# Performance work log

Hardware: AMD Instinct MI355X
Metric: run time of the kernel (lower is better)

The kernel has to match this reference:

```python
import jax, jax.numpy as jnp
import numpy as np

D_IN, L, D, K, N_CLASSES = 1024, 512, 384, 1, 2

def setup_inputs() -> dict:
    key = jax.random.key(0)
    ks = jax.random.split(key, 11)
    x = jax.random.normal(ks[0], (2, 40000, D_IN), dtype=jnp.float32)
    # Linear params stored as [in, out]; xavier-normal-ish scale
    def w(k, i, o):
        return jax.random.normal(k, (i, o), dtype=jnp.float32) * jnp.sqrt(2.0 / (i + o))
    return {
        "x": x,
        "Wf": w(ks[1], D_IN, L), "bf": jnp.zeros((L,), jnp.float32),
        "Wa": w(ks[2], L, D),    "ba": jnp.zeros((D,), jnp.float32),
        "Wb": w(ks[3], L, D),    "bb": jnp.zeros((D,), jnp.float32),
        "Wc": w(ks[4], D, K),    "bc": jnp.zeros((K,), jnp.float32),
        "Wcls": w(ks[5], L * K, N_CLASSES), "bcls": jnp.zeros((N_CLASSES,), jnp.float32),
    }

def reference(x, Wf, bf, Wa, ba, Wb, bb, Wc, bc, Wcls, bcls):
    # feature embed: Linear + ReLU  (mil_norm=None -> Identity norms)
    h = jax.nn.relu(jnp.einsum('bnd,de->bne', x, Wf) + bf)   # [B,N,L]
    # gated attention
    a = jnp.tanh(jnp.einsum('bnl,ld->bnd', h, Wa) + ba)      # [B,N,D]
    g = jax.nn.sigmoid(jnp.einsum('bnl,ld->bnd', h, Wb) + bb)
    s = jnp.einsum('bnd,dk->bnk', a * g, Wc) + bc            # [B,N,K]
    A = jax.nn.softmax(jnp.swapaxes(s, -1, -2), axis=-1)     # [B,K,N]
    pooled = jnp.einsum('bkn,bnl->bkl', A, h)                # [B,K,L]
    logits = jnp.squeeze(pooled, 1) @ Wcls + bcls            # [B,n_classes]
    return logits
```

## Files before the change

### kernel.cpp

```cpp
#include <hip/hip_runtime.h>
#include <cstdint>

typedef _Float16 f16;
typedef __attribute__((ext_vector_type(8))) _Float16 half8;
typedef __attribute__((ext_vector_type(4))) float floatx4;

#define NB      40000
#define M_TOTAL 80000
#define DIN     1024
#define LDIM    512
#define NBLK    1250
#define BPB     625

__global__ void k_prep(const float* __restrict__ Wf, const float* __restrict__ Wa,
                       const float* __restrict__ Wb,
                       f16* __restrict__ packedF, f16* __restrict__ packedAB)
{
    const int gid = blockIdx.x * 256 + threadIdx.x;
    if (gid < 65536) {
        const int lq = gid & 3, n = (gid >> 2) & 511, kb = gid >> 11;
        const int kbase = kb * 32 + lq * 8;
        half8 v;
        #pragma unroll
        for (int j = 0; j < 8; ++j) v[j] = (f16)Wf[(kbase + j) * 512 + n];
        *(half8*)&packedF[(long)gid * 8] = v;
    } else if (gid < 65536 + 49152) {
        const int g = gid - 65536;
        const int kb = g / 3072;
        const int rem = g - kb * 3072;
        const int c = rem >> 2, lq = rem & 3;
        const int d = ((c >> 5) << 4) + (c & 15);
        const int type = (c >> 4) & 1;
        const float* src = type ? Wb : Wa;
        const int kbase = kb * 32 + lq * 8;
        half8 v;
        #pragma unroll
        for (int j = 0; j < 8; ++j) v[j] = (f16)src[(kbase + j) * 384 + d];
        *(half8*)&packedAB[(long)g * 8] = v;
    }
}

__device__ inline float fast_sigmoid(float xx) { return 1.0f / (1.0f + __expf(-xx)); }
__device__ inline float fast_tanh(float xx) {
    float e = __expf(-2.0f * fabsf(xx));
    float r = (1.0f - e) / (1.0f + e);
    return xx >= 0.0f ? r : -r;
}

__global__ __launch_bounds__(512, 4) void k_fused(
    const float* __restrict__ x, const f16* __restrict__ packedF,
    const f16* __restrict__ packedAB,
    const float* __restrict__ bf, const float* __restrict__ ba,
    const float* __restrict__ bb, const float* __restrict__ Wc,
    float* __restrict__ partial_pool, float* __restrict__ partial_denom)
{
    __shared__ __align__(16) f16 Hs[64][520];
    __shared__ __align__(16) f16 As[64][72];
    __shared__ float wbuf[64];
    const int tid = threadIdx.x;
    const int w = tid >> 6, lane = tid & 63, lr = lane & 15, lq = lane >> 4;
    const long row0 = (long)blockIdx.x * 64;
    const int sr = tid >> 3, st = (tid & 7) * 8;
    const float* xp = x + (row0 + sr) * DIN + st;
    if (tid < 64) wbuf[tid] = 0.0f;

    floatx4 acc[4][4] = {};
    float4 xa = *(const float4*)xp;
    float4 xb = *(const float4*)(xp + 4);
    for (int kt = 0; kt < 16; ++kt) {
        __syncthreads();
        {
            half8 hv;
            hv[0]=(f16)xa.x; hv[1]=(f16)xa.y; hv[2]=(f16)xa.z; hv[3]=(f16)xa.w;
            hv[4]=(f16)xb.x; hv[5]=(f16)xb.y; hv[6]=(f16)xb.z; hv[7]=(f16)xb.w;
            *(half8*)&As[sr][st] = hv;
        }
        __syncthreads();
        if (kt < 15) {
            const float* q = xp + (kt + 1) * 64;
            xa = *(const float4*)q;
            xb = *(const float4*)(q + 4);
        }
        #pragma unroll
        for (int kq = 0; kq < 2; ++kq) {
            const int kb = kt * 2 + kq;
            half8 bfr[4];
            #pragma unroll
            for (int tj = 0; tj < 4; ++tj)
                bfr[tj] = *(const half8*)&packedF[(long)((kb * 512 + w * 64 + tj * 16 + lr) << 5) + lq * 8];
            half8 af[4];
            #pragma unroll
            for (int ti = 0; ti < 4; ++ti)
                af[ti] = *(const half8*)&As[ti * 16 + lr][kq * 32 + lq * 8];
            #pragma unroll
            for (int tj = 0; tj < 4; ++tj)
                #pragma unroll
                for (int ti = 0; ti < 4; ++ti)
                    acc[ti][tj] = __builtin_amdgcn_mfma_f32_16x16x32_f16(af[ti], bfr[tj], acc[ti][tj], 0, 0, 0);
        }
    }
    #pragma unroll
    for (int tj = 0; tj < 4; ++tj) {
        const int col = w * 64 + tj * 16 + lr;
        const float bias = bf[col];
        #pragma unroll
        for (int ti = 0; ti < 4; ++ti)
            #pragma unroll
            for (int r = 0; r < 4; ++r)
                Hs[ti * 16 + lq * 4 + r][col] = (f16)fmaxf(acc[ti][tj][r] + bias, 0.0f);
    }
    __syncthreads();

    floatx4 acc2[4][6] = {};
    for (int kb = 0; kb < 16; ++kb) {
        half8 af[4];
        #pragma unroll
        for (int ti = 0; ti < 4; ++ti)
            af[ti] = *(const half8*)&Hs[ti * 16 + lr][kb * 32 + lq * 8];
        #pragma unroll
        for (int tj = 0; tj < 6; ++tj) {
            half8 bfr = *(const half8*)&packedAB[(long)((kb * 768 + w * 96 + tj * 16 + lr) << 5) + lq * 8];
            #pragma unroll
            for (int ti = 0; ti < 4; ++ti)
                acc2[ti][tj] = __builtin_amdgcn_mfma_f32_16x16x32_f16(af[ti], bfr, acc2[ti][tj], 0, 0, 0);
        }
    }
    float sp[4][4] = {};
    #pragma unroll
    for (int u = 0; u < 3; ++u) {
        const int d = w * 48 + u * 16 + lr;
        const float biasA = ba[d], biasB = bb[d], wcv = Wc[d];
        #pragma unroll
        for (int ti = 0; ti < 4; ++ti)
            #pragma unroll
            for (int r = 0; r < 4; ++r) {
                const float av = fast_tanh(acc2[ti][2 * u][r] + biasA);
                const float gv = fast_sigmoid(acc2[ti][2 * u + 1][r] + biasB);
                sp[ti][r] += av * gv * wcv;
            }
    }
    #pragma unroll
    for (int m = 1; m < 16; m <<= 1)
        #pragma unroll
        for (int ti = 0; ti < 4; ++ti)
            #pragma unroll
            for (int r = 0; r < 4; ++r)
                sp[ti][r] += __shfl_xor(sp[ti][r], m, 64);
    if (lr == 0) {
        #pragma unroll
        for (int ti = 0; ti < 4; ++ti)
            #pragma unroll
            for (int r = 0; r < 4; ++r)
                atomicAdd(&wbuf[ti * 16 + lq * 4 + r], sp[ti][r]);
    }
    __syncthreads();
    if (tid < 64) wbuf[tid] = __expf(wbuf[tid]);
    __syncthreads();

    {
        const int c = tid;
        float pacc = 0.0f;
        #pragma unroll 8
        for (int n = 0; n < 64; ++n)
            pacc += wbuf[n] * (float)Hs[n][c];
        partial_pool[(long)blockIdx.x * 512 + c] = pacc;
    }
    if (w == 0) {
        float dsum = wbuf[lane];
        #pragma unroll
        for (int o = 32; o > 0; o >>= 1) dsum += __shfl_xor(dsum, o, 64);
        if (lane == 0) partial_denom[blockIdx.x] = dsum;
    }
}

__global__ __launch_bounds__(512) void k_reduce(
    const float* __restrict__ pp, const float* __restrict__ pd,
    const float* __restrict__ Wcls, const float* __restrict__ bcls,
    float* __restrict__ out)
{
    __shared__ float pooled[512];
    __shared__ float dsh[8];
    const int b = blockIdx.x, tid = threadIdx.x;
    float acc = 0.0f;
    const float* base = pp + (long)b * BPB * 512 + tid;
    for (int i = 0; i < BPB; ++i) acc += base[(long)i * 512];
    pooled[tid] = acc;
    float d = 0.0f;
    for (int i = tid; i < BPB; i += 512) d += pd[b * BPB + i];
    #pragma unroll
    for (int o = 32; o > 0; o >>= 1) d += __shfl_xor(d, o, 64);
    if ((tid & 63) == 0) dsh[tid >> 6] = d;
    __syncthreads();
    const float denom = dsh[0] + dsh[1] + dsh[2] + dsh[3] + dsh[4] + dsh[5] + dsh[6] + dsh[7];
    if (tid < 128) {
        const int cls = tid >> 6, ln = tid & 63;
        float sum = 0.0f;
        #pragma unroll
        for (int t = 0; t < 8; ++t)
            sum += pooled[t * 64 + ln] * Wcls[(t * 64 + ln) * 2 + cls];
        #pragma unroll
        for (int o = 32; o > 0; o >>= 1) sum += __shfl_xor(sum, o, 64);
        if (ln == 0) out[b * 2 + cls] = sum / denom + bcls[cls];
    }
}

extern "C" void kernel_launch(void* const* d_in, const int* in_sizes, int n_in,
                              void* d_out, int out_size, void* d_ws, size_t ws_size,
                              hipStream_t stream)
{
    const float* x    = (const float*)d_in[0];
    const float* Wf   = (const float*)d_in[1];
    const float* bf   = (const float*)d_in[2];
    const float* Wa   = (const float*)d_in[3];
    const float* ba   = (const float*)d_in[4];
    const float* Wb   = (const float*)d_in[5];
    const float* bb   = (const float*)d_in[6];
    const float* Wc   = (const float*)d_in[7];
    const float* Wcls = (const float*)d_in[9];
    const float* bcls = (const float*)d_in[10];
    float* out = (float*)d_out;

    char* w = (char*)d_ws;
    f16*   packedF  = (f16*)(w);
    f16*   packedAB = (f16*)(w + 1048576);
    float* ppool    = (float*)(w + 1835008);
    float* pdenom   = (float*)(w + 4395008);

    k_prep  <<<448, 256, 0, stream>>>(Wf, Wa, Wb, packedF, packedAB);
    k_fused <<<NBLK, 512, 0, stream>>>(x, packedF, packedAB, bf, ba, bb, Wc, ppool, pdenom);
    k_reduce<<<2, 512, 0, stream>>>(ppool, pdenom, Wcls, bcls, out);
}
```

Baseline: 712.9 us.

## Swizzle LDS tiles, widen K-step to 128, split final reduction into two stages

Replaces padded LDS arrays with XOR-swizzled layouts for the x tile and the H tile to avoid bank conflicts without padding. The x staging tile doubles to 128 columns, halving the number of barrier-separated K iterations. wbuf now aliases the A tile. The single 2-block final reduction over 625 partials per batch is split into a 32-block first pass and a small second pass, adding a launch in exchange for more parallelism. The second-stage buffers reuse the packedF workspace region, which k_fused no longer needs by then.

Result: faster. 690.3 us (-3.2%).

```diff
diff --git a/kernel.cpp b/kernel.cpp
--- a/kernel.cpp
+++ b/kernel.cpp
@@ -11,6 +11,8 @@
 #define LDIM    512
 #define NBLK    1250
 #define BPB     625
+#define NCHUNK  16
+#define RCHUNK  40
 
 __global__ void k_prep(const float* __restrict__ Wf, const float* __restrict__ Wa,
                        const float* __restrict__ Wb,
@@ -54,36 +56,46 @@
     const float* __restrict__ bb, const float* __restrict__ Wc,
     float* __restrict__ partial_pool, float* __restrict__ partial_denom)
 {
-    __shared__ __align__(16) f16 Hs[64][520];
-    __shared__ __align__(16) f16 As[64][72];
-    __shared__ float wbuf[64];
+    __shared__ __align__(16) f16 Hs[64][512];
+    __shared__ __align__(16) f16 As[64][128];
+    float* wbuf = (float*)&As[0][0];
+
     const int tid = threadIdx.x;
     const int w = tid >> 6, lane = tid & 63, lr = lane & 15, lq = lane >> 4;
     const long row0 = (long)blockIdx.x * 64;
-    const int sr = tid >> 3, st = (tid & 7) * 8;
-    const float* xp = x + (row0 + sr) * DIN + st;
-    if (tid < 64) wbuf[tid] = 0.0f;
+    const int sr = tid >> 3;
+    const int sc = (tid & 7) << 4;
+    const int swzw = (sr & 7) << 3;
+    const int swzr = (lr & 7) << 3;
+    const float* xp = x + (row0 + sr) * DIN + sc;
 
     floatx4 acc[4][4] = {};
-    float4 xa = *(const float4*)xp;
-    float4 xb = *(const float4*)(xp + 4);
-    for (int kt = 0; kt < 16; ++kt) {
+    float4 xr0 = *(const float4*)xp;
+    float4 xr1 = *(const float4*)(xp + 4);
+    float4 xr2 = *(const float4*)(xp + 8);
+    float4 xr3 = *(const float4*)(xp + 12);
+    for (int kt = 0; kt < 8; ++kt) {
+        if (kt) __syncthreads();
+        {
+            half8 v0, v1;
+            v0[0]=(f16)xr0.x; v0[1]=(f16)xr0.y; v0[2]=(f16)xr0.z; v0[3]=(f16)xr0.w;
+            v0[4]=(f16)xr1.x; v0[5]=(f16)xr1.y; v0[6]=(f16)xr1.z; v0[7]=(f16)xr1.w;
+            v1[0]=(f16)xr2.x; v1[1]=(f16)xr2.y; v1[2]=(f16)xr2.z; v1[3]=(f16)xr2.w;
+            v1[4]=(f16)xr3.x; v1[5]=(f16)xr3.y; v1[6]=(f16)xr3.z; v1[7]=(f16)xr3.w;
+            *(half8*)&As[sr][sc ^ swzw] = v0;
+            *(half8*)&As[sr][(sc + 8) ^ swzw] = v1;
+        }
         __syncthreads();
-        {
-            half8 hv;
-            hv[0]=(f16)xa.x; hv[1]=(f16)xa.y; hv[2]=(f16)xa.z; hv[3]=(f16)xa.w;
-            hv[4]=(f16)xb.x; hv[5]=(f16)xb.y; hv[6]=(f16)xb.z; hv[7]=(f16)xb.w;
-            *(half8*)&As[sr][st] = hv;
-        }
-        __syncthreads();
-        if (kt < 15) {
-            const float* q = xp + (kt + 1) * 64;
-            xa = *(const float4*)q;
-            xb = *(const float4*)(q + 4);
-        }
-        #pragma unroll
-        for (int kq = 0; kq < 2; ++kq) {
-            const int kb = kt * 2 + kq;
+        if (kt < 7) {
+            const float* q = xp + (kt + 1) * 128;
+            xr0 = *(const float4*)q;
+            xr1 = *(const float4*)(q + 4);
+            xr2 = *(const float4*)(q + 8);
+            xr3 = *(const float4*)(q + 12);
+        }
+        #pragma unroll
+        for (int kq = 0; kq < 4; ++kq) {
+            const int kb = kt * 4 + kq;
             half8 bfr[4];
             #pragma unroll
             for (int tj = 0; tj < 4; ++tj)
@@ -91,7 +103,7 @@
             half8 af[4];
             #pragma unroll
             for (int ti = 0; ti < 4; ++ti)
-                af[ti] = *(const half8*)&As[ti * 16 + lr][kq * 32 + lq * 8];
+                af[ti] = *(const half8*)&As[ti * 16 + lr][(kq * 32 + lq * 8) ^ swzr];
             #pragma unroll
             for (int tj = 0; tj < 4; ++tj)
                 #pragma unroll
@@ -106,9 +118,13 @@
         #pragma unroll
         for (int ti = 0; ti < 4; ++ti)
             #pragma unroll
-            for (int r = 0; r < 4; ++r)
-                Hs[ti * 16 + lq * 4 + r][col] = (f16)fmaxf(acc[ti][tj][r] + bias, 0.0f);
-    }
+            for (int r = 0; r < 4; ++r) {
+                const int row = ti * 16 + lq * 4 + r;
+                Hs[row][col ^ ((row & 7) << 3)] = (f16)fmaxf(acc[ti][tj][r] + bias, 0.0f);
+            }
+    }
+    __syncthreads();
+    if (tid < 64) wbuf[tid] = 0.0f;
     __syncthreads();
 
     floatx4 acc2[4][6] = {};
@@ -116,7 +132,7 @@
         half8 af[4];
         #pragma unroll
         for (int ti = 0; ti < 4; ++ti)
-            af[ti] = *(const half8*)&Hs[ti * 16 + lr][kb * 32 + lq * 8];
+            af[ti] = *(const half8*)&Hs[ti * 16 + lr][(kb * 32 + lq * 8) ^ swzr];
         #pragma unroll
         for (int tj = 0; tj < 6; ++tj) {
             half8 bfr = *(const half8*)&packedAB[(long)((kb * 768 + w * 96 + tj * 16 + lr) << 5) + lq * 8];
@@ -162,7 +178,7 @@
         float pacc = 0.0f;
         #pragma unroll 8
         for (int n = 0; n < 64; ++n)
-            pacc += wbuf[n] * (float)Hs[n][c];
+            pacc += wbuf[n] * (float)Hs[n][c ^ ((n & 7) << 3)];
         partial_pool[(long)blockIdx.x * 512 + c] = pacc;
     }
     if (w == 0) {
@@ -173,8 +189,32 @@
     }
 }
 
-__global__ __launch_bounds__(512) void k_reduce(
+__global__ __launch_bounds__(512) void k_reduce1(
     const float* __restrict__ pp, const float* __restrict__ pd,
+    float* __restrict__ pp2, float* __restrict__ pd2)
+{
+    __shared__ float dsh[8];
+    const int b = blockIdx.x >> 4, chunk = blockIdx.x & 15;
+    const int tid = threadIdx.x;
+    const int r0 = chunk * RCHUNK;
+    const int rows = (BPB - r0 < RCHUNK) ? (BPB - r0) : RCHUNK;
+    const float* base = pp + ((long)b * BPB + r0) * 512 + tid;
+    float acc = 0.0f;
+    for (int i = 0; i < rows; ++i) acc += base[(long)i * 512];
+    pp2[((long)b * NCHUNK + chunk) * 512 + tid] = acc;
+    float d = 0.0f;
+    for (int i = tid; i < rows; i += 512) d += pd[b * BPB + r0 + i];
+    #pragma unroll
+    for (int o = 32; o > 0; o >>= 1) d += __shfl_xor(d, o, 64);
+    if ((tid & 63) == 0) dsh[tid >> 6] = d;
+    __syncthreads();
+    if (tid == 0)
+        pd2[b * NCHUNK + chunk] = dsh[0] + dsh[1] + dsh[2] + dsh[3]
+                                + dsh[4] + dsh[5] + dsh[6] + dsh[7];
+}
+
+__global__ __launch_bounds__(512) void k_reduce2(
+    const float* __restrict__ pp2, const float* __restrict__ pd2,
     const float* __restrict__ Wcls, const float* __restrict__ bcls,
     float* __restrict__ out)
 {
@@ -182,11 +222,11 @@
     __shared__ float dsh[8];
     const int b = blockIdx.x, tid = threadIdx.x;
     float acc = 0.0f;
-    const float* base = pp + (long)b * BPB * 512 + tid;
-    for (int i = 0; i < BPB; ++i) acc += base[(long)i * 512];
+    const float* base = pp2 + (long)b * NCHUNK * 512 + tid;
+    #pragma unroll
+    for (int i = 0; i < NCHUNK; ++i) acc += base[i * 512];
     pooled[tid] = acc;
-    float d = 0.0f;
-    for (int i = tid; i < BPB; i += 512) d += pd[b * BPB + i];
+    float d = (tid < NCHUNK) ? pd2[b * NCHUNK + tid] : 0.0f;
     #pragma unroll
     for (int o = 32; o > 0; o >>= 1) d += __shfl_xor(d, o, 64);
     if ((tid & 63) == 0) dsh[tid >> 6] = d;
@@ -225,8 +265,11 @@
     f16*   packedAB = (f16*)(w + 1048576);
     float* ppool    = (float*)(w + 1835008);
     float* pdenom   = (float*)(w + 4395008);
-
-    k_prep  <<<448, 256, 0, stream>>>(Wf, Wa, Wb, packedF, packedAB);
-    k_fused <<<NBLK, 512, 0, stream>>>(x, packedF, packedAB, bf, ba, bb, Wc, ppool, pdenom);
-    k_reduce<<<2, 512, 0, stream>>>(ppool, pdenom, Wcls, bcls, out);
-}
+    float* pp2      = (float*)(w);
+    float* pd2      = (float*)(w + 65536);
+
+    k_prep   <<<448, 256, 0, stream>>>(Wf, Wa, Wb, packedF, packedAB);
+    k_fused  <<<NBLK, 512, 0, stream>>>(x, packedF, packedAB, bf, ba, bb, Wc, ppool, pdenom);
+    k_reduce1<<<32, 512, 0, stream>>>(ppool, pdenom, pp2, pd2);
+    k_reduce2<<<2, 512, 0, stream>>>(pp2, pd2, Wcls, bcls, out);
+}
```
